# Kernel optimization log

Hardware: AMD Instinct MI355X
Metric: run time of the kernel (lower is better)

Reference implementation:

```python
import jax, jax.numpy as jnp
import numpy as np

D_MODEL = 1024
HEADS = 16
D_K = D_MODEL // HEADS
B, S = 4, 2048


def setup_inputs() -> dict:
    key = jax.random.key(0)
    ks = jax.random.split(key, 12)
    xav = float(np.sqrt(6.0 / (D_MODEL + D_MODEL)))  # xavier_uniform bound
    inp = {
        "query": jax.random.normal(ks[0], (B, S, D_MODEL), jnp.float32),
        "key": jax.random.normal(ks[1], (B, S, D_MODEL), jnp.float32),
        "value": jax.random.normal(ks[2], (B, S, D_MODEL), jnp.float32),
        # causal mask, broadcast over batch and heads: [1,1,S,S]
        "mask": jnp.tril(jnp.ones((S, S), jnp.int32))[None, None],
        "Wq": jax.random.uniform(ks[3], (D_MODEL, D_MODEL), jnp.float32, -xav, xav),
        "bq": jnp.zeros((D_MODEL,), jnp.float32),
        "Wk": jax.random.uniform(ks[4], (D_MODEL, D_MODEL), jnp.float32, -xav, xav),
        "bk": jnp.zeros((D_MODEL,), jnp.float32),
        "Wv": jax.random.uniform(ks[5], (D_MODEL, D_MODEL), jnp.float32, -xav, xav),
        "bv": jnp.zeros((D_MODEL,), jnp.float32),
        "Wo": jax.random.uniform(ks[6], (D_MODEL, D_MODEL), jnp.float32, -xav, xav),
        "bo": jnp.zeros((D_MODEL,), jnp.float32),
    }
    return inp


def reference(query, key, value, mask, Wq, bq, Wk, bk, Wv, bv, Wo, bo):
    b, s, d = query.shape
    # torch Linear: y = x @ W.T + b, W is [out, in]
    Q = (jnp.einsum("bsd,ed->bse", query, Wq) + bq).reshape(b, s, HEADS, D_K).transpose(0, 2, 1, 3)
    K = (jnp.einsum("bsd,ed->bse", key, Wk) + bk).reshape(b, -1, HEADS, D_K).transpose(0, 2, 1, 3)
    V = (jnp.einsum("bsd,ed->bse", value, Wv) + bv).reshape(b, -1, HEADS, D_K).transpose(0, 2, 1, 3)
    scale = 1.0 / jnp.sqrt(jnp.asarray(D_K, query.dtype))
    scores = jnp.einsum("bhqd,bhkd->bhqk", Q, K) * scale  # [B,H,S,S]
    scores = jnp.where(mask == 0, -jnp.inf, scores)
    attn = jax.nn.softmax(scores, axis=-1)
    attn = jnp.where(jnp.isnan(attn), jnp.zeros_like(attn), attn)  # nan-fix as in source
    out = jnp.einsum("bhqk,bhkd->bhqd", attn, V)
    out = out.transpose(0, 2, 1, 3).reshape(b, s, d)
    return jnp.einsum("bsd,ed->bse", out, Wo) + bo
```

## Files before the change

kernel.cpp:

```cpp
#include <hip/hip_runtime.h>
#include <hip/hip_bf16.h>

#define DM 1024
#define NHEADS 16
#define DKH 64
#define BATCH 4
#define SEQ 2048
#define MROWS (BATCH*SEQ)

typedef __attribute__((ext_vector_type(8))) short bf16x8;
typedef __attribute__((ext_vector_type(4))) short bf16x4;
typedef __attribute__((ext_vector_type(4))) float f32x4;

#if __has_builtin(__builtin_amdgcn_exp2f)
#define EXP2(x) __builtin_amdgcn_exp2f(x)
#else
#define EXP2(x) exp2f(x)
#endif

__device__ __forceinline__ unsigned short f2bf(float f){
  unsigned u = __float_as_uint(f);
  u += 0x7fffu + ((u >> 16) & 1u);
  return (unsigned short)(u >> 16);
}

__device__ __forceinline__ unsigned pk2bf(float lo, float hi){
  union { __hip_bfloat162 h; unsigned u; } c;
  c.h = __float22bfloat162_rn(make_float2(lo, hi));
  return c.u;
}

__device__ __forceinline__ bf16x8 cvtA8(float4 a, float4 b){
  union { unsigned u[4]; bf16x8 v; } r;
  r.u[0] = pk2bf(a.x, a.y);
  r.u[1] = pk2bf(a.z, a.w);
  r.u[2] = pk2bf(b.x, b.y);
  r.u[3] = pk2bf(b.z, b.w);
  return r.v;
}

__device__ __forceinline__ void gload16(const unsigned short* g, unsigned short* l){
  __builtin_amdgcn_global_load_lds((const __attribute__((address_space(1))) void*)g,
                                   (__attribute__((address_space(3))) void*)l, 16, 0, 0);
}

struct ConvArgs { const float* src[4]; unsigned short* dst[4]; };

__global__ __launch_bounds__(256) void conv_w(ConvArgs a){
  const int t = blockIdx.x >> 10;
  const int boff = blockIdx.x & 1023;
  const float* __restrict__ src = a.src[t];
  unsigned short* __restrict__ dst = a.dst[t];
  const int i = (boff * 256 + threadIdx.x) * 4;
  const float4 v = *reinterpret_cast<const float4*>(src + i);
  ushort4 o;
  o.x = f2bf(v.x); o.y = f2bf(v.y); o.z = f2bf(v.z); o.w = f2bf(v.w);
  *reinterpret_cast<ushort4*>(dst + i) = o;
}

template<int MODE, int AFP32>
__global__ __launch_bounds__(256)
void gemm_bt(const void* __restrict__ Av, const unsigned short* __restrict__ Bw,
             const float* __restrict__ bias, void* __restrict__ out, float scale)
{
  const int K = 1024;
  __shared__ short a_sh[128*64];
  __shared__ short b_sh[128*64];
  const int tid  = threadIdx.x;
  const int lane = tid & 63;
  const int wid  = tid >> 6;
  const int wm = wid >> 1, wn = wid & 1;
  const int lin = blockIdx.x;
  const int xcd = lin & 7;
  const int i9  = lin >> 3;
  const int tileM = (8*xcd + (i9 >> 3)) * 128;
  const int tileN = (i9 & 7) * 128;

  f32x4 acc[4][4];
  #pragma unroll
  for (int i = 0; i < 4; i++)
    #pragma unroll
    for (int j = 0; j < 4; j++)
      acc[i][j] = (f32x4){0.f,0.f,0.f,0.f};

  const int lr = lane & 15;
  const int lg = lane >> 4;
  const int r8 = lane >> 3, c8 = lane & 7;
  const int srow = 8*wid + r8;
  const int sgrp = (c8 ^ r8) * 8;

  for (int k0 = 0; k0 < K; k0 += 64){
    bf16x8 ra[4];
    if constexpr (AFP32){
      const float* Af = (const float*)Av;
      #pragma unroll
      for (int i = 0; i < 4; i++){
        int v   = tid + 256*i;
        int row = v >> 3;
        int cg  = v & 7;
        const float4 f0 = *reinterpret_cast<const float4*>(Af + (size_t)(tileM+row)*K + k0 + cg*8);
        const float4 f1 = *reinterpret_cast<const float4*>(Af + (size_t)(tileM+row)*K + k0 + cg*8 + 4);
        ra[i] = cvtA8(f0, f1);
      }
    }
    __syncthreads();
    #pragma unroll
    for (int j = 0; j < 4; j++){
      gload16(Bw + (size_t)(tileN + srow + 32*j)*K + k0 + sgrp,
              (unsigned short*)&b_sh[(8*wid + 32*j)*64]);
    }
    if constexpr (AFP32){
      #pragma unroll
      for (int i = 0; i < 4; i++){
        int v   = tid + 256*i;
        int row = v >> 3;
        int cg  = v & 7;
        *reinterpret_cast<bf16x8*>(&a_sh[row*64 + ((cg ^ (row & 7)) * 8)]) = ra[i];
      }
    } else {
      const unsigned short* Ab = (const unsigned short*)Av;
      #pragma unroll
      for (int j = 0; j < 4; j++){
        gload16(Ab + (size_t)(tileM + srow + 32*j)*K + k0 + sgrp,
                (unsigned short*)&a_sh[(8*wid + 32*j)*64]);
      }
    }
    __syncthreads();

    #pragma unroll
    for (int kk = 0; kk < 64; kk += 32){
      bf16x8 af[4], bfr[4];
      const int g0 = lg + (kk >> 3);
      #pragma unroll
      for (int fm = 0; fm < 4; fm++){
        int row = wm*64 + fm*16 + lr;
        af[fm] = *reinterpret_cast<const bf16x8*>(&a_sh[row*64 + ((g0 ^ (row & 7)) * 8)]);
      }
      #pragma unroll
      for (int fn = 0; fn < 4; fn++){
        int row = wn*64 + fn*16 + lr;
        bfr[fn] = *reinterpret_cast<const bf16x8*>(&b_sh[row*64 + ((g0 ^ (row & 7)) * 8)]);
      }
      #pragma unroll
      for (int fm = 0; fm < 4; fm++)
        #pragma unroll
        for (int fn = 0; fn < 4; fn++)
          acc[fm][fn] = __builtin_amdgcn_mfma_f32_16x16x32_bf16(af[fm], bfr[fn], acc[fm][fn], 0, 0, 0);
    }
  }

  #pragma unroll
  for (int fm = 0; fm < 4; fm++){
    #pragma unroll
    for (int fn = 0; fn < 4; fn++){
      #pragma unroll
      for (int r = 0; r < 4; r++){
        int m = tileM + wm*64 + fm*16 + lg*4 + r;
        int n = tileN + wn*64 + fn*16 + lr;
        float val = acc[fm][fn][r] + bias[n];
        if (MODE == 0){
          val *= scale;
          int b = m >> 11, s = m & 2047, h = n >> 6, d = n & 63;
          ((unsigned short*)out)[(((size_t)(b*NHEADS + h)*SEQ + s)*DKH + d)] = f2bf(val);
        } else if (MODE == 1){
          int b = m >> 11, s = m & 2047, h = n >> 6, d = n & 63;
          ((unsigned short*)out)[(((size_t)(b*NHEADS + h)*DKH + d)*SEQ + s)] = f2bf(val);
        } else {
          ((float*)out)[(size_t)m*DM + n] = val;
        }
      }
    }
  }
}

__global__ __launch_bounds__(512, 4)
void attn_kernel(const unsigned short* __restrict__ Q, const unsigned short* __restrict__ Kb,
                 const unsigned short* __restrict__ Vt, unsigned short* __restrict__ Oout)
{
  __shared__ unsigned short k_sh[2][128*64];
  __shared__ unsigned short v_sh[2][64*128];
  const int lane = threadIdx.x & 63;
  const int w    = threadIdx.x >> 6;
  const int lr = lane & 15, grp = lane >> 4;
  const int bh = blockIdx.x;
  const int y  = (int)blockIdx.y;
  const int hiT = 15 - y;
  const int myTile = (w < 4) ? hiT : y;
  const int qb0 = myTile * 128;
  const int qw0 = qb0 + (w & 3) * 32;
  const int b = bh >> 4, h = bh & 15;
  const size_t kbase = (size_t)bh * SEQ * DKH;
  const size_t vbase = (size_t)bh * DKH * SEQ;

  const int r8 = lane >> 3, c8 = lane & 7;
  const size_t offK0 = (size_t)(16*w + r8)*DKH     + (size_t)((c8 ^ r8) * 8);
  const size_t offK1 = (size_t)(16*w + 8 + r8)*DKH + (size_t)((c8 ^ r8) * 8);
  const int ldsK0 = (16*w)*64, ldsK1 = (16*w + 8)*64;
  const int r4 = lane >> 4, c16 = lane & 15;
  const size_t offV0 = (size_t)(8*w + r4)*SEQ     + (size_t)((c16 ^ r4) * 8);
  const size_t offV1 = (size_t)(8*w + 4 + r4)*SEQ + (size_t)((c16 ^ (4 + r4)) * 8);
  const int ldsV0 = (8*w)*128, ldsV1 = (8*w + 4)*128;

  bf16x8 qf[2][2];
  #pragma unroll
  for (int qg = 0; qg < 2; qg++){
    size_t off = kbase + (size_t)(qw0 + qg*16 + lr)*DKH + grp*8;
    qf[qg][0] = *reinterpret_cast<const bf16x8*>(Q + off);
    qf[qg][1] = *reinterpret_cast<const bf16x8*>(Q + off + 32);
  }

  bf16x4 ones4;
  ones4[0] = (short)0x3F80; ones4[1] = (short)0x3F80;
  ones4[2] = (short)0x3F80; ones4[3] = (short)0x3F80;

  float mrun[2] = {-__builtin_inff(), -__builtin_inff()};
  f32x4 ls[2];
  f32x4 o[2][4];
  #pragma unroll
  for (int qg = 0; qg < 2; qg++){
    ls[qg] = (f32x4){0.f,0.f,0.f,0.f};
    #pragma unroll
    for (int dc = 0; dc < 4; dc++) o[qg][dc] = (f32x4){0.f,0.f,0.f,0.f};
  }

  const int nkb = hiT + 1;

#define STAGE(kb_, bf_) do { \
    gload16(Kb + kbase + (size_t)(kb_)*8192 + offK0, (unsigned short*)&k_sh[bf_][ldsK0]); \
    gload16(Kb + kbase + (size_t)(kb_)*8192 + offK1, (unsigned short*)&k_sh[bf_][ldsK1]); \
    gload16(Vt + vbase + (size_t)(kb_)*128  + offV0, (unsigned short*)&v_sh[bf_][ldsV0]); \
    gload16(Vt + vbase + (size_t)(kb_)*128  + offV1, (unsigned short*)&v_sh[bf_][ldsV1]); \
  } while(0)

  STAGE(0, 0);
  __syncthreads();

  for (int kb = 0; kb < nkb; kb++){
    const int buf = kb & 1;
    if (kb + 1 < nkb) STAGE(kb + 1, buf ^ 1);

    #pragma unroll
    for (int kh = 0; kh < 2; kh++){
      const int base_k = kb*128 + kh*64;
      if (base_k <= qw0 + 31){
        const unsigned short* ks = &k_sh[buf][kh*4096];
        const unsigned short* vs = v_sh[buf];
        const bool act0 = (base_k <= qw0 + 15);

        bf16x4 pb[2][4];
        #pragma unroll
        for (int qg = 0; qg < 2; qg++){
          if (qg == 0 && !act0) continue;
          f32x4 st[4];
          __builtin_amdgcn_s_setprio(1);
          #pragma unroll
          for (int ksub = 0; ksub < 4; ksub++){
            int rowk = ksub*16 + lr;
            bf16x8 kf0 = *reinterpret_cast<const bf16x8*>(&ks[rowk*64 + ((grp ^ (rowk & 7)) * 8)]);
            bf16x8 kf1 = *reinterpret_cast<const bf16x8*>(&ks[rowk*64 + (((4 + grp) ^ (rowk & 7)) * 8)]);
            f32x4 s = (f32x4){0.f,0.f,0.f,0.f};
            s = __builtin_amdgcn_mfma_f32_16x16x32_bf16(kf0, qf[qg][0], s, 0, 0, 0);
            s = __builtin_amdgcn_mfma_f32_16x16x32_bf16(kf1, qf[qg][1], s, 0, 0, 0);
            st[ksub] = s;
          }
          __builtin_amdgcn_s_setprio(0);

          const int qgb = qw0 + qg*16;
          if (base_k + 63 > qgb){
            #pragma unroll
            for (int ksub = 0; ksub < 4; ksub++)
              #pragma unroll
              for (int r = 0; r < 4; r++){
                int kg = base_k + ksub*16 + grp*4 + r;
                if (kg > qgb + lr) st[ksub][r] = -__builtin_inff();
              }
          }
          float mt = fmaxf(fmaxf(st[0][0], st[0][1]), fmaxf(st[0][2], st[0][3]));
          #pragma unroll
          for (int ksub = 1; ksub < 4; ksub++){
            mt = fmaxf(mt, fmaxf(fmaxf(st[ksub][0], st[ksub][1]),
                                 fmaxf(st[ksub][2], st[ksub][3])));
          }
          mt = fmaxf(mt, __shfl_xor(mt, 16));
          mt = fmaxf(mt, __shfl_xor(mt, 32));
          if (__any(mt > mrun[qg] + 8.f)){
            const float mold = mrun[qg];
            const float mnew = fmaxf(mold, mt);
            const float corr = EXP2(mold - mnew);
            mrun[qg] = mnew;
            #pragma unroll
            for (int dc = 0; dc < 4; dc++){
              o[qg][dc][0] *= corr; o[qg][dc][1] *= corr;
              o[qg][dc][2] *= corr; o[qg][dc][3] *= corr;
            }
            ls[qg][0] *= corr;
          }
          const float m = mrun[qg];
          #pragma unroll
          for (int ksub = 0; ksub < 4; ksub++){
            float p0 = EXP2(st[ksub][0] - m);
            float p1 = EXP2(st[ksub][1] - m);
            float p2 = EXP2(st[ksub][2] - m);
            float p3 = EXP2(st[ksub][3] - m);
            union { unsigned u[2]; bf16x4 v; } pk;
            pk.u[0] = pk2bf(p0, p1);
            pk.u[1] = pk2bf(p2, p3);
            pb[qg][ksub] = pk.v;
          }
        }

        __builtin_amdgcn_s_setprio(1);
        #pragma unroll
        for (int ksub = 0; ksub < 4; ksub++){
          const int cg16 = kh*8 + ksub*2 + (grp >> 1);
          #pragma unroll
          for (int dc = 0; dc < 4; dc++){
            int rowd = dc*16 + lr;
            bf16x4 vf = *reinterpret_cast<const bf16x4*>(
                &vs[rowd*128 + ((cg16 ^ (rowd & 7)) * 8) + (grp & 1)*4]);
            if (act0) o[0][dc] = __builtin_amdgcn_mfma_f32_16x16x16bf16_1k(vf, pb[0][ksub], o[0][dc], 0, 0, 0);
            o[1][dc] = __builtin_amdgcn_mfma_f32_16x16x16bf16_1k(vf, pb[1][ksub], o[1][dc], 0, 0, 0);
          }
          if (act0) ls[0] = __builtin_amdgcn_mfma_f32_16x16x16bf16_1k(ones4, pb[0][ksub], ls[0], 0, 0, 0);
          ls[1] = __builtin_amdgcn_mfma_f32_16x16x16bf16_1k(ones4, pb[1][ksub], ls[1], 0, 0, 0);
        }
        __builtin_amdgcn_s_setprio(0);
      }
    }
    __syncthreads();
  }
#undef STAGE

  #pragma unroll
  for (int qg = 0; qg < 2; qg++){
    float inv = 1.0f / ls[qg][0];
    int qglob = qw0 + qg*16 + lr;
    size_t ob = ((size_t)(b*SEQ + qglob))*DM + h*DKH;
    #pragma unroll
    for (int dc = 0; dc < 4; dc++){
      ushort4 pk;
      pk.x = f2bf(o[qg][dc][0]*inv);
      pk.y = f2bf(o[qg][dc][1]*inv);
      pk.z = f2bf(o[qg][dc][2]*inv);
      pk.w = f2bf(o[qg][dc][3]*inv);
      *reinterpret_cast<ushort4*>(&Oout[ob + dc*16 + grp*4]) = pk;
    }
  }
}

extern "C" void kernel_launch(void* const* d_in, const int* in_sizes, int n_in,
                              void* d_out, int out_size, void* d_ws, size_t ws_size,
                              hipStream_t stream) {
  const float* query = (const float*)d_in[0];
  const float* key   = (const float*)d_in[1];
  const float* value = (const float*)d_in[2];
  const float* Wq = (const float*)d_in[4];
  const float* bq = (const float*)d_in[5];
  const float* Wk = (const float*)d_in[6];
  const float* bk = (const float*)d_in[7];
  const float* Wv = (const float*)d_in[8];
  const float* bv = (const float*)d_in[9];
  const float* Wo = (const float*)d_in[10];
  const float* bo = (const float*)d_in[11];
  float* out = (float*)d_out;

  char* ws = (char*)d_ws;
  const size_t SZ_X = (size_t)MROWS * DM * 2;
  const size_t SZ_W = (size_t)DM * DM * 2;
  unsigned short* wqb = (unsigned short*)(ws + 0);
  unsigned short* wkb = (unsigned short*)(ws + SZ_W);
  unsigned short* wvb = (unsigned short*)(ws + 2*SZ_W);
  unsigned short* wob = (unsigned short*)(ws + 3*SZ_W);
  unsigned short* Qb   = (unsigned short*)(ws + 4*SZ_W);
  unsigned short* Kbuf = (unsigned short*)(ws + 4*SZ_W + SZ_X);
  unsigned short* Vt   = (unsigned short*)(ws + 4*SZ_W + 2*SZ_X);
  unsigned short* attO = (unsigned short*)(ws + 4*SZ_W + 3*SZ_X);

  ConvArgs ca;
  ca.src[0] = Wq; ca.src[1] = Wk; ca.src[2] = Wv; ca.src[3] = Wo;
  ca.dst[0] = wqb; ca.dst[1] = wkb; ca.dst[2] = wvb; ca.dst[3] = wob;
  conv_w<<<4096, 256, 0, stream>>>(ca);

  const int NBLK = (MROWS/128) * (DM/128);
  const float qscale = 0.125f * 1.4426950408889634f;
  gemm_bt<1,1><<<NBLK, 256, 0, stream>>>(value, wvb, bv, (void*)Vt,   1.0f);
  gemm_bt<0,1><<<NBLK, 256, 0, stream>>>(query, wqb, bq, (void*)Qb,   qscale);
  gemm_bt<0,1><<<NBLK, 256, 0, stream>>>(key,   wkb, bk, (void*)Kbuf, 1.0f);

  attn_kernel<<<dim3(64, 8), 512, 0, stream>>>(Qb, Kbuf, Vt, attO);

  gemm_bt<2,0><<<NBLK, 256, 0, stream>>>(attO, wob, bo, (void*)out, 1.0f);
}
```

Measured before the change: 193.1 us.

## Rewrite attention inner loop with 32x32x16 MFMA tiles and VALU row sums

Switches the flash-attention kernel from 16x16 MFMA fragments to 32x32x16 bf16 MFMAs. Each wave now processes 32 queries per 32-key chunk, and the P fragment is rebuilt for the PV product with cross-half lane shuffles. The softmax denominator is now summed with VALU adds plus one shuffle, replacing the extra MFMA against a ones vector. Launch bounds drop from 4 to 2 blocks per SM to give room for the larger 16-float accumulators, which may lower occupancy and latency hiding.

```diff
diff --git a/kernel.cpp b/kernel.cpp
--- a/kernel.cpp
+++ b/kernel.cpp
@@ -11,6 +11,7 @@
 typedef __attribute__((ext_vector_type(8))) short bf16x8;
 typedef __attribute__((ext_vector_type(4))) short bf16x4;
 typedef __attribute__((ext_vector_type(4))) float f32x4;
+typedef __attribute__((ext_vector_type(16))) float f32x16;
 
 #if __has_builtin(__builtin_amdgcn_exp2f)
 #define EXP2(x) __builtin_amdgcn_exp2f(x)
@@ -173,7 +174,7 @@
   }
 }
 
-__global__ __launch_bounds__(512, 4)
+__global__ __launch_bounds__(512, 2)
 void attn_kernel(const unsigned short* __restrict__ Q, const unsigned short* __restrict__ Kb,
                  const unsigned short* __restrict__ Vt, unsigned short* __restrict__ Oout)
 {
@@ -181,13 +182,16 @@
   __shared__ unsigned short v_sh[2][64*128];
   const int lane = threadIdx.x & 63;
   const int w    = threadIdx.x >> 6;
-  const int lr = lane & 15, grp = lane >> 4;
+  const int q32  = lane & 31;
+  const int hi   = lane >> 5;
+  const int l7   = lane & 7;
   const int bh = blockIdx.x;
   const int y  = (int)blockIdx.y;
   const int hiT = 15 - y;
   const int myTile = (w < 4) ? hiT : y;
   const int qb0 = myTile * 128;
   const int qw0 = qb0 + (w & 3) * 32;
+  const int qglob = qw0 + q32;
   const int b = bh >> 4, h = bh & 15;
   const size_t kbase = (size_t)bh * SEQ * DKH;
   const size_t vbase = (size_t)bh * DKH * SEQ;
@@ -201,27 +205,20 @@
   const size_t offV1 = (size_t)(8*w + 4 + r4)*SEQ + (size_t)((c16 ^ (4 + r4)) * 8);
   const int ldsV0 = (8*w)*128, ldsV1 = (8*w + 4)*128;
 
-  bf16x8 qf[2][2];
-  #pragma unroll
-  for (int qg = 0; qg < 2; qg++){
-    size_t off = kbase + (size_t)(qw0 + qg*16 + lr)*DKH + grp*8;
-    qf[qg][0] = *reinterpret_cast<const bf16x8*>(Q + off);
-    qf[qg][1] = *reinterpret_cast<const bf16x8*>(Q + off + 32);
-  }
-
-  bf16x4 ones4;
-  ones4[0] = (short)0x3F80; ones4[1] = (short)0x3F80;
-  ones4[2] = (short)0x3F80; ones4[3] = (short)0x3F80;
-
-  float mrun[2] = {-__builtin_inff(), -__builtin_inff()};
-  f32x4 ls[2];
-  f32x4 o[2][4];
-  #pragma unroll
-  for (int qg = 0; qg < 2; qg++){
-    ls[qg] = (f32x4){0.f,0.f,0.f,0.f};
-    #pragma unroll
-    for (int dc = 0; dc < 4; dc++) o[qg][dc] = (f32x4){0.f,0.f,0.f,0.f};
-  }
+  bf16x8 qf[4];
+  #pragma unroll
+  for (int dblk = 0; dblk < 4; dblk++){
+    qf[dblk] = *reinterpret_cast<const bf16x8*>(Q + kbase + (size_t)qglob*DKH + dblk*16 + hi*8);
+  }
+
+  float mrun = -__builtin_inff();
+  float llocal = 0.f;
+  f32x16 o0, o1;
+  #pragma unroll
+  for (int r = 0; r < 16; r++){ o0[r] = 0.f; o1[r] = 0.f; }
+  f32x16 zero16;
+  #pragma unroll
+  for (int r = 0; r < 16; r++) zero16[r] = 0.f;
 
   const int nkb = hiT + 1;
 
@@ -239,90 +236,91 @@
     const int buf = kb & 1;
     if (kb + 1 < nkb) STAGE(kb + 1, buf ^ 1);
 
-    #pragma unroll
-    for (int kh = 0; kh < 2; kh++){
-      const int base_k = kb*128 + kh*64;
+    const unsigned short* ks = k_sh[buf];
+    const unsigned short* vs = v_sh[buf];
+
+    #pragma unroll
+    for (int c = 0; c < 4; c++){
+      const int base_k = kb*128 + c*32;
       if (base_k <= qw0 + 31){
-        const unsigned short* ks = &k_sh[buf][kh*4096];
-        const unsigned short* vs = v_sh[buf];
-        const bool act0 = (base_k <= qw0 + 15);
-
-        bf16x4 pb[2][4];
-        #pragma unroll
-        for (int qg = 0; qg < 2; qg++){
-          if (qg == 0 && !act0) continue;
-          f32x4 st[4];
-          __builtin_amdgcn_s_setprio(1);
+        f32x16 st;
+        __builtin_amdgcn_s_setprio(1);
+        {
+          bf16x8 kf0 = *reinterpret_cast<const bf16x8*>(&ks[(c*32 + q32)*64 + (((0*2 + hi) ^ l7) * 8)]);
+          st = __builtin_amdgcn_mfma_f32_32x32x16_bf16(kf0, qf[0], zero16, 0, 0, 0);
+        }
+        #pragma unroll
+        for (int dblk = 1; dblk < 4; dblk++){
+          bf16x8 kf = *reinterpret_cast<const bf16x8*>(&ks[(c*32 + q32)*64 + (((dblk*2 + hi) ^ l7) * 8)]);
+          st = __builtin_amdgcn_mfma_f32_32x32x16_bf16(kf, qf[dblk], st, 0, 0, 0);
+        }
+        __builtin_amdgcn_s_setprio(0);
+
+        if (base_k + 31 > qw0){
           #pragma unroll
-          for (int ksub = 0; ksub < 4; ksub++){
-            int rowk = ksub*16 + lr;
-            bf16x8 kf0 = *reinterpret_cast<const bf16x8*>(&ks[rowk*64 + ((grp ^ (rowk & 7)) * 8)]);
-            bf16x8 kf1 = *reinterpret_cast<const bf16x8*>(&ks[rowk*64 + (((4 + grp) ^ (rowk & 7)) * 8)]);
-            f32x4 s = (f32x4){0.f,0.f,0.f,0.f};
-            s = __builtin_amdgcn_mfma_f32_16x16x32_bf16(kf0, qf[qg][0], s, 0, 0, 0);
-            s = __builtin_amdgcn_mfma_f32_16x16x32_bf16(kf1, qf[qg][1], s, 0, 0, 0);
-            st[ksub] = s;
+          for (int r = 0; r < 16; r++){
+            int kg = base_k + (r & 3) + 8*(r >> 2) + 4*hi;
+            if (kg > qglob) st[r] = -__builtin_inff();
           }
-          __builtin_amdgcn_s_setprio(0);
-
-          const int qgb = qw0 + qg*16;
-          if (base_k + 63 > qgb){
-            #pragma unroll
-            for (int ksub = 0; ksub < 4; ksub++)
-              #pragma unroll
-              for (int r = 0; r < 4; r++){
-                int kg = base_k + ksub*16 + grp*4 + r;
-                if (kg > qgb + lr) st[ksub][r] = -__builtin_inff();
-              }
+        }
+
+        float mt = st[0];
+        #pragma unroll
+        for (int r = 1; r < 16; r++) mt = fmaxf(mt, st[r]);
+        mt = fmaxf(mt, __shfl_xor(mt, 32));
+
+        if (__any(mt > mrun + 8.f)){
+          const float mnew = fmaxf(mrun, mt);
+          const float corr = EXP2(mrun - mnew);
+          mrun = mnew;
+          #pragma unroll
+          for (int r = 0; r < 16; r++){ o0[r] *= corr; o1[r] *= corr; }
+          llocal *= corr;
+        }
+
+        float p[16];
+        #pragma unroll
+        for (int r = 0; r < 16; r++) p[r] = EXP2(st[r] - mrun);
+        {
+          float s0 = (p[0]+p[1]) + (p[2]+p[3]);
+          float s1 = (p[4]+p[5]) + (p[6]+p[7]);
+          float s2 = (p[8]+p[9]) + (p[10]+p[11]);
+          float s3 = (p[12]+p[13]) + (p[14]+p[15]);
+          llocal += (s0+s1) + (s2+s3);
+        }
+        unsigned pkA0 = pk2bf(p[0],  p[1]),  pkA1 = pk2bf(p[2],  p[3]);
+        unsigned pkB0 = pk2bf(p[4],  p[5]),  pkB1 = pk2bf(p[6],  p[7]);
+        unsigned pkC0 = pk2bf(p[8],  p[9]),  pkC1 = pk2bf(p[10], p[11]);
+        unsigned pkD0 = pk2bf(p[12], p[13]), pkD1 = pk2bf(p[14], p[15]);
+        unsigned xA0 = __shfl_xor(pkA0, 32), xA1 = __shfl_xor(pkA1, 32);
+        unsigned xB0 = __shfl_xor(pkB0, 32), xB1 = __shfl_xor(pkB1, 32);
+        unsigned xC0 = __shfl_xor(pkC0, 32), xC1 = __shfl_xor(pkC1, 32);
+        unsigned xD0 = __shfl_xor(pkD0, 32), xD1 = __shfl_xor(pkD1, 32);
+        const bool lo = (hi == 0);
+        union { unsigned u[4]; bf16x8 v; } f0, f1;
+        f0.u[0] = lo ? pkA0 : xB0;
+        f0.u[1] = lo ? pkA1 : xB1;
+        f0.u[2] = lo ? xA0  : pkB0;
+        f0.u[3] = lo ? xA1  : pkB1;
+        f1.u[0] = lo ? pkC0 : xD0;
+        f1.u[1] = lo ? pkC1 : xD1;
+        f1.u[2] = lo ? xC0  : pkD0;
+        f1.u[3] = lo ? xC1  : pkD1;
+
+        __builtin_amdgcn_s_setprio(1);
+        #pragma unroll
+        for (int k16 = 0; k16 < 2; k16++){
+          bf16x8 fr = k16 ? f1.v : f0.v;
+          {
+            bf16x8 vf = *reinterpret_cast<const bf16x8*>(
+                &vs[(0*32 + q32)*128 + (((c*4 + k16*2 + hi) ^ l7) * 8)]);
+            o0 = __builtin_amdgcn_mfma_f32_32x32x16_bf16(vf, fr, o0, 0, 0, 0);
           }
-          float mt = fmaxf(fmaxf(st[0][0], st[0][1]), fmaxf(st[0][2], st[0][3]));
-          #pragma unroll
-          for (int ksub = 1; ksub < 4; ksub++){
-            mt = fmaxf(mt, fmaxf(fmaxf(st[ksub][0], st[ksub][1]),
-                                 fmaxf(st[ksub][2], st[ksub][3])));
+          {
+            bf16x8 vf = *reinterpret_cast<const bf16x8*>(
+                &vs[(1*32 + q32)*128 + (((c*4 + k16*2 + hi) ^ l7) * 8)]);
+            o1 = __builtin_amdgcn_mfma_f32_32x32x16_bf16(vf, fr, o1, 0, 0, 0);
           }
-          mt = fmaxf(mt, __shfl_xor(mt, 16));
-          mt = fmaxf(mt, __shfl_xor(mt, 32));
-          if (__any(mt > mrun[qg] + 8.f)){
-            const float mold = mrun[qg];
-            const float mnew = fmaxf(mold, mt);
-            const float corr = EXP2(mold - mnew);
-            mrun[qg] = mnew;
-            #pragma unroll
-            for (int dc = 0; dc < 4; dc++){
-              o[qg][dc][0] *= corr; o[qg][dc][1] *= corr;
-              o[qg][dc][2] *= corr; o[qg][dc][3] *= corr;
-            }
-            ls[qg][0] *= corr;
-          }
-          const float m = mrun[qg];
-          #pragma unroll
-          for (int ksub = 0; ksub < 4; ksub++){
-            float p0 = EXP2(st[ksub][0] - m);
-            float p1 = EXP2(st[ksub][1] - m);
-            float p2 = EXP2(st[ksub][2] - m);
-            float p3 = EXP2(st[ksub][3] - m);
-            union { unsigned u[2]; bf16x4 v; } pk;
-            pk.u[0] = pk2bf(p0, p1);
-            pk.u[1] = pk2bf(p2, p3);
-            pb[qg][ksub] = pk.v;
-          }
-        }
-
-        __builtin_amdgcn_s_setprio(1);
-        #pragma unroll
-        for (int ksub = 0; ksub < 4; ksub++){
-          const int cg16 = kh*8 + ksub*2 + (grp >> 1);
-          #pragma unroll
-          for (int dc = 0; dc < 4; dc++){
-            int rowd = dc*16 + lr;
-            bf16x4 vf = *reinterpret_cast<const bf16x4*>(
-                &vs[rowd*128 + ((cg16 ^ (rowd & 7)) * 8) + (grp & 1)*4]);
-            if (act0) o[0][dc] = __builtin_amdgcn_mfma_f32_16x16x16bf16_1k(vf, pb[0][ksub], o[0][dc], 0, 0, 0);
-            o[1][dc] = __builtin_amdgcn_mfma_f32_16x16x16bf16_1k(vf, pb[1][ksub], o[1][dc], 0, 0, 0);
-          }
-          if (act0) ls[0] = __builtin_amdgcn_mfma_f32_16x16x16bf16_1k(ones4, pb[0][ksub], ls[0], 0, 0, 0);
-          ls[1] = __builtin_amdgcn_mfma_f32_16x16x16bf16_1k(ones4, pb[1][ksub], ls[1], 0, 0, 0);
         }
         __builtin_amdgcn_s_setprio(0);
       }
@@ -331,20 +329,19 @@
   }
 #undef STAGE
 
-  #pragma unroll
-  for (int qg = 0; qg < 2; qg++){
-    float inv = 1.0f / ls[qg][0];
-    int qglob = qw0 + qg*16 + lr;
-    size_t ob = ((size_t)(b*SEQ + qglob))*DM + h*DKH;
-    #pragma unroll
-    for (int dc = 0; dc < 4; dc++){
-      ushort4 pk;
-      pk.x = f2bf(o[qg][dc][0]*inv);
-      pk.y = f2bf(o[qg][dc][1]*inv);
-      pk.z = f2bf(o[qg][dc][2]*inv);
-      pk.w = f2bf(o[qg][dc][3]*inv);
-      *reinterpret_cast<ushort4*>(&Oout[ob + dc*16 + grp*4]) = pk;
-    }
+  const float l = llocal + __shfl_xor(llocal, 32);
+  const float inv = 1.0f / l;
+  size_t ob = ((size_t)(b*SEQ + qglob))*DM + h*DKH;
+  #pragma unroll
+  for (int g = 0; g < 4; g++){
+    ushort4 pk;
+    pk.x = f2bf(o0[4*g+0]*inv); pk.y = f2bf(o0[4*g+1]*inv);
+    pk.z = f2bf(o0[4*g+2]*inv); pk.w = f2bf(o0[4*g+3]*inv);
+    *reinterpret_cast<ushort4*>(&Oout[ob + 8*g + 4*hi]) = pk;
+    ushort4 pk2;
+    pk2.x = f2bf(o1[4*g+0]*inv); pk2.y = f2bf(o1[4*g+1]*inv);
+    pk2.z = f2bf(o1[4*g+2]*inv); pk2.w = f2bf(o1[4*g+3]*inv);
+    *reinterpret_cast<ushort4*>(&Oout[ob + 32 + 8*g + 4*hi]) = pk2;
   }
 }
 
```

Result: faster. 188.5 us, median of 2 (-2.4%).
